# Performance work log

Hardware: AMD Instinct MI355X
Metric: run time of the kernel (lower is better)

The kernel has to match this reference:

```python
import jax, jax.numpy as jnp
import numpy as np

B_BOUND = 3.0
K = 10
SCALE_DIM = 8
TOTAL_DIM = 16
HID = 50
N = 262144
TD = TOTAL_DIM - SCALE_DIM  # transform_dim


def setup_inputs() -> dict:
    key = jax.random.key(0)
    ks = jax.random.split(key, 7)
    s = 0.1  # small init so softmax/softplus params stay well-conditioned
    return {
        "x": jax.random.normal(ks[0], (N, TOTAL_DIM), dtype=jnp.float32),
        "w0": s * jax.random.normal(ks[1], (SCALE_DIM, HID), dtype=jnp.float32),
        "b0": jnp.zeros((HID,), jnp.float32),
        "w1": s * jax.random.normal(ks[2], (HID, HID), dtype=jnp.float32),
        "b1": jnp.zeros((HID,), jnp.float32),
        "ww": s * jax.random.normal(ks[3], (HID, TD * K), dtype=jnp.float32),
        "bw": jnp.zeros((TD * K,), jnp.float32),
        "wh": s * jax.random.normal(ks[4], (HID, TD * K), dtype=jnp.float32),
        "bh": jnp.zeros((TD * K,), jnp.float32),
        "wd": s * jax.random.normal(ks[5], (HID, TD * (K - 1)), dtype=jnp.float32),
        "bd": jnp.zeros((TD * (K - 1),), jnp.float32),
    }


def _spline_forward(x, w0, b0, w1, b1, ww, bw, wh, bh, wd, bd):
    B = B_BOUND
    zd = x[:, :SCALE_DIM]          # conditioner input [N, d]
    u = x[:, SCALE_DIM:]           # values to transform [N, D]
    n, D = u.shape

    h = jnp.tanh(zd @ w0 + b0)
    h = jnp.tanh(h @ w1 + b1)

    theta_w = jax.nn.softmax((2.0 * B * (h @ ww + bw)).reshape(n, D, K), axis=-1)
    theta_h = jax.nn.softmax((2.0 * B * (h @ wh + bh)).reshape(n, D, K), axis=-1)
    theta_d = jax.nn.softplus((h @ wd + bd).reshape(n, D, K - 1))

    # Bin edges in [-B, B] via cumsum of normalized widths/heights
    xe = jnp.concatenate(
        [jnp.full((n, D, 1), -B, u.dtype), -B + 2.0 * B * jnp.cumsum(theta_w, axis=-1)], axis=-1)  # [n,D,K+1]
    ye = jnp.concatenate(
        [jnp.full((n, D, 1), -B, u.dtype), -B + 2.0 * B * jnp.cumsum(theta_h, axis=-1)], axis=-1)
    # Knot derivatives: boundary derivatives fixed to 1 (linear tails)
    ones = jnp.ones((n, D, 1), u.dtype)
    d = jnp.concatenate([ones, theta_d, ones], axis=-1)  # [n,D,K+1]

    widths = xe[..., 1:] - xe[..., :-1]
    heights = ye[..., 1:] - ye[..., :-1]

    inside = (u > -B) & (u < B)
    uc = jnp.clip(u, -B, B)
    # per-element bin search
    idx = jnp.clip(jnp.sum((uc[..., None] >= xe[..., :-1]).astype(jnp.int32), axis=-1) - 1, 0, K - 1)
    idx = idx[..., None]
    take = lambda a: jnp.take_along_axis(a, idx, axis=-1)[..., 0]

    xk, yk = take(xe[..., :-1]), take(ye[..., :-1])
    wk, hk = take(widths), take(heights)
    dk, dk1 = take(d[..., :-1]), take(d[..., 1:])

    sk = hk / wk
    xi = (uc - xk) / wk
    om = 1.0 - xi
    denom = sk + (dk1 + dk - 2.0 * sk) * xi * om
    y = yk + hk * (sk * xi * xi + dk * xi * om) / denom
    logdet = 2.0 * jnp.log(sk) + jnp.log(dk1 * xi * xi + 2.0 * sk * xi * om + dk * om * om) - 2.0 * jnp.log(denom)

    zD = jnp.where(inside, y, u)
    ld = jnp.where(inside, logdet, 0.0)
    return jnp.concatenate([zd, zD], axis=1), jnp.sum(ld)


def reference(x, w0, b0, w1, b1, ww, bw, wh, bh, wd, bd):
    return _spline_forward(x, w0, b0, w1, b1, ww, bw, wh, bh, wd, bd)
```

## Files before the change

kernel.cpp:

```cpp
#include <hip/hip_runtime.h>

#define NROWS 262144
#define KK 10
#define BB 3.0f
#define SROW 132
#define HS 84
#define SEGF16 (16 * SROW)
#define SENT 0.54132485f

typedef _Float16 v8h __attribute__((ext_vector_type(8)));
typedef _Float16 v4h __attribute__((ext_vector_type(4)));
typedef float v4f __attribute__((ext_vector_type(4)));

#define W0_OFF 0
#define W1_OFF 256
#define WC_OFF 768
#define FRAG_TOTAL 2816
#define SLOTS_OFF (FRAG_TOTAL * 4)

#if __has_builtin(__builtin_amdgcn_exp2f)
__device__ __forceinline__ float ex2(float x) { return __builtin_amdgcn_exp2f(x); }
#else
__device__ __forceinline__ float ex2(float x) { return __expf(0.6931471805599453f * x); }
#endif
#if __has_builtin(__builtin_amdgcn_rcpf)
__device__ __forceinline__ float frcp(float x) { return __builtin_amdgcn_rcpf(x); }
#else
__device__ __forceinline__ float frcp(float x) { return __fdividef(1.0f, x); }
#endif

#define LOG2E 1.4426950408889634f
#define C6 (6.0f * LOG2E)
#define CT (2.0f * LOG2E)

__device__ __forceinline__ float fast_tanh(float a) {
    const float e = ex2(CT * a);
    return fmaf(-2.0f, frcp(e + 1.0f), 1.0f);
}

__device__ __forceinline__ float softplus1(float v) {
    return fmaxf(v, 0.0f) + __logf(1.0f + ex2(-LOG2E * fabsf(v)));
}

__device__ __forceinline__ void spline_task(
    const _Float16* __restrict__ sg, int base, float ud, int g, int d,
    float* __restrict__ out, float& ldacc)
{
    float vals[32];
    #pragma unroll
    for (int blk = 0; blk < 8; ++blk) {
        const v4h p = *(const v4h*)&sg[base + blk * 4];
        vals[4 * blk + 0] = (float)p[0];
        vals[4 * blk + 1] = (float)p[1];
        vals[4 * blk + 2] = (float)p[2];
        vals[4 * blk + 3] = (float)p[3];
    }

    float mw = vals[0];
    #pragma unroll
    for (int i = 1; i < KK; ++i) mw = fmaxf(mw, vals[i]);
    const float mw8 = mw * C6;
    float sw = 0.0f;
    #pragma unroll
    for (int i = 0; i < KK; ++i) { vals[i] = ex2(fmaf(vals[i], C6, -mw8)); sw += vals[i]; }
    const float invw = frcp(sw);

    float mh = vals[10];
    #pragma unroll
    for (int i = 1; i < KK; ++i) mh = fmaxf(mh, vals[10 + i]);
    const float mh8 = mh * C6;
    float sh = 0.0f;
    #pragma unroll
    for (int i = 0; i < KK; ++i) { vals[10 + i] = ex2(fmaf(vals[10 + i], C6, -mh8)); sh += vals[10 + i]; }
    const float invh = frcp(sh);

    const float uc = fminf(fmaxf(ud, -BB), BB);
    const bool inside = (ud > -BB) && (ud < BB);

    float cw = 0.0f, ch = 0.0f;
    float xprev = -BB, yprev = -BB, rprev = SENT;
    float xk = -BB, yk = -BB, wk = 1.0f, hk2 = 1.0f, rdk = SENT, rdk1 = SENT;
    #pragma unroll
    for (int i = 0; i < KK; ++i) {
        cw += vals[i] * invw;
        ch += vals[10 + i] * invh;
        const float xnext = fmaf(6.0f, cw, -BB);
        const float ynext = fmaf(6.0f, ch, -BB);
        const float rnext = (i == KK - 1) ? SENT : vals[20 + i];
        const bool c = (i == 0) || (uc >= xprev);
        if (c) { xk = xprev; yk = yprev; wk = xnext - xprev; hk2 = ynext - yprev; rdk = rprev; rdk1 = rnext; }
        xprev = xnext; yprev = ynext; rprev = rnext;
    }
    const float dk = softplus1(rdk);
    const float dk1 = softplus1(rdk1);

    const float rwk = frcp(wk);
    const float sk = hk2 * rwk;
    const float xi = (uc - xk) * rwk;
    const float om = 1.0f - xi;
    const float denom = sk + (dk1 + dk - 2.0f * sk) * xi * om;
    const float rden = frcp(denom);
    const float ynum = sk * xi * xi + dk * xi * om;
    const float yv = yk + hk2 * ynum * rden;
    const float larg = dk1 * xi * xi + 2.0f * sk * xi * om + dk * om * om;
    const float ldet = __logf(sk * sk * larg * rden * rden);

    out[g * 16 + 8 + d] = inside ? yv : ud;
    ldacc += inside ? ldet : 0.0f;
}

__global__ __launch_bounds__(256) void nsf_prep(
    const float* __restrict__ w0, const float* __restrict__ b0,
    const float* __restrict__ w1, const float* __restrict__ b1,
    const float* __restrict__ ww, const float* __restrict__ bw,
    const float* __restrict__ wh, const float* __restrict__ bh,
    const float* __restrict__ wd, const float* __restrict__ bd,
    v8h* __restrict__ wsv, float* __restrict__ wsf)
{
    const int t = blockIdx.x * 256 + threadIdx.x;
    if (t < 64) wsf[SLOTS_OFF + t] = 0.0f;
    if (t >= FRAG_TOTAL) return;

    v8h v;
    #pragma unroll
    for (int j = 0; j < 8; ++j) v[j] = (_Float16)0.0f;

    if (t < W1_OFF) {
        const int tile = t >> 6, lane = t & 63, q = lane >> 4, n = tile * 16 + (lane & 15);
        if (n < 50) {
            #pragma unroll
            for (int j = 0; j < 8; ++j) {
                const int k = q * 8 + j;
                if (k < 8)       v[j] = (_Float16)w0[k * 50 + n];
                else if (k == 8) v[j] = (_Float16)b0[n];
            }
        }
    } else if (t < WC_OFF) {
        int p = t - W1_OFF;
        const int step = p >> 8; p &= 255;
        const int tile = p >> 6, lane = p & 63, q = lane >> 4, n = tile * 16 + (lane & 15);
        if (n < 50) {
            #pragma unroll
            for (int j = 0; j < 8; ++j) {
                const int k = step * 32 + q * 8 + j;
                if (k < 50)       v[j] = (_Float16)w1[k * 50 + n];
                else if (k == 50) v[j] = (_Float16)b1[n];
            }
        }
    } else {
        int p = t - WC_OFF;
        const int step = p >> 10; p &= 1023;
        const int tile = p >> 6, lane = p & 63, q = lane >> 4;
        const int cp = tile * 16 + (lane & 15);
        const int d = cp >> 5, jj = cp & 31;
        #pragma unroll
        for (int j = 0; j < 8; ++j) {
            const int k = step * 32 + q * 8 + j;
            float val = 0.0f;
            if (k < 50) {
                if (jj < 10)      val = ww[k * 80 + d * 10 + jj];
                else if (jj < 20) val = wh[k * 80 + d * 10 + (jj - 10)];
                else if (jj < 29) val = wd[k * 72 + d * 9 + (jj - 20)];
            } else if (k == 50) {
                if (jj < 10)      val = bw[d * 10 + jj];
                else if (jj < 20) val = bh[d * 10 + (jj - 10)];
                else if (jj < 29) val = bd[d * 9 + (jj - 20)];
            }
            v[j] = (_Float16)val;
        }
    }
    wsv[t] = v;
}

__global__ __launch_bounds__(128) void nsf_main_v8(
    const float* __restrict__ x,
    const v8h* __restrict__ wsv,
    float* __restrict__ out, float* __restrict__ slots)
{
    __shared__ __align__(16) _Float16 smem[4 * SEGF16];
    const int w = threadIdx.x >> 6;
    const int lane = threadIdx.x & 63;
    const int q = lane >> 4, l15 = lane & 15;
    _Float16* segA = &smem[(2 * w) * SEGF16];
    _Float16* segB = &smem[(2 * w + 1) * SEGF16];
    const int waveId = blockIdx.x * 2 + w;
    const int R0 = waveId * 32;

    const float4* xv = (const float4*)x;
    float4* ov = (float4*)out;

    const float uA0 = x[(R0 + l15) * 16 + 8 + q];
    const float uA1 = x[(R0 + l15) * 16 + 12 + q];
    const float uB0 = x[(R0 + 16 + l15) * 16 + 8 + q];
    const float uB1 = x[(R0 + 16 + l15) * 16 + 12 + q];

    {
        const int gg = R0 + (lane >> 1);
        const int part = lane & 1;
        ov[gg * 4 + part] = xv[gg * 4 + part];
    }

    v8h aA, aB;
    #pragma unroll
    for (int j = 0; j < 8; ++j) { aA[j] = (_Float16)0.0f; aB[j] = (_Float16)0.0f; }
    if (lane < 16) {
        const float4 f0 = xv[(R0 + lane) * 4 + 0];
        const float4 f1 = xv[(R0 + lane) * 4 + 1];
        aA[0] = (_Float16)f0.x; aA[1] = (_Float16)f0.y; aA[2] = (_Float16)f0.z; aA[3] = (_Float16)f0.w;
        aA[4] = (_Float16)f1.x; aA[5] = (_Float16)f1.y; aA[6] = (_Float16)f1.z; aA[7] = (_Float16)f1.w;
        const float4 g0 = xv[(R0 + 16 + lane) * 4 + 0];
        const float4 g1 = xv[(R0 + 16 + lane) * 4 + 1];
        aB[0] = (_Float16)g0.x; aB[1] = (_Float16)g0.y; aB[2] = (_Float16)g0.z; aB[3] = (_Float16)g0.w;
        aB[4] = (_Float16)g1.x; aB[5] = (_Float16)g1.y; aB[6] = (_Float16)g1.z; aB[7] = (_Float16)g1.w;
    }
    if (q == 1) { aA[0] = (_Float16)1.0f; aB[0] = (_Float16)1.0f; }

    #pragma unroll
    for (int t = 0; t < 4; ++t) {
        const v8h b = wsv[W0_OFF + t * 64 + lane];
        v4f cA = __builtin_amdgcn_mfma_f32_16x16x32_f16(b, aA, (v4f)(0.0f), 0, 0, 0);
        v4f cB = __builtin_amdgcn_mfma_f32_16x16x32_f16(b, aB, (v4f)(0.0f), 0, 0, 0);
        v4h pA, pB;
        #pragma unroll
        for (int rg = 0; rg < 4; ++rg) {
            pA[rg] = (_Float16)fast_tanh(cA[rg]);
            pB[rg] = (_Float16)fast_tanh(cB[rg]);
        }
        const int o = l15 * HS + t * 16 + q * 4;
        *(v4h*)&segA[o] = pA;
        *(v4h*)&segB[o] = pB;
    }

    v8h A0A, A1A, A0B, A1B;
    {
        const int o0 = l15 * HS + q * 8;
        const int o1 = l15 * HS + 32 + q * 8;
        const v4h a0l = *(const v4h*)&segA[o0], a0h = *(const v4h*)&segA[o0 + 4];
        const v4h a1l = *(const v4h*)&segA[o1], a1h = *(const v4h*)&segA[o1 + 4];
        const v4h b0l = *(const v4h*)&segB[o0], b0h = *(const v4h*)&segB[o0 + 4];
        const v4h b1l = *(const v4h*)&segB[o1], b1h = *(const v4h*)&segB[o1 + 4];
        #pragma unroll
        for (int j = 0; j < 4; ++j) {
            A0A[j] = a0l[j]; A0A[4 + j] = a0h[j];
            A1A[j] = a1l[j]; A1A[4 + j] = a1h[j];
            A0B[j] = b0l[j]; A0B[4 + j] = b0h[j];
            A1B[j] = b1l[j]; A1B[4 + j] = b1h[j];
        }
    }
    if (q == 2) { A1A[2] = (_Float16)1.0f; A1B[2] = (_Float16)1.0f; }
    #pragma unroll
    for (int t = 0; t < 4; ++t) {
        const v8h bf0 = wsv[W1_OFF + t * 64 + lane];
        const v8h bf1 = wsv[W1_OFF + 256 + t * 64 + lane];
        v4f cA = __builtin_amdgcn_mfma_f32_16x16x32_f16(bf0, A0A, (v4f)(0.0f), 0, 0, 0);
        cA = __builtin_amdgcn_mfma_f32_16x16x32_f16(bf1, A1A, cA, 0, 0, 0);
        v4f cB = __builtin_amdgcn_mfma_f32_16x16x32_f16(bf0, A0B, (v4f)(0.0f), 0, 0, 0);
        cB = __builtin_amdgcn_mfma_f32_16x16x32_f16(bf1, A1B, cB, 0, 0, 0);
        v4h pA, pB;
        #pragma unroll
        for (int rg = 0; rg < 4; ++rg) {
            pA[rg] = (_Float16)fast_tanh(cA[rg]);
            pB[rg] = (_Float16)fast_tanh(cB[rg]);
        }
        const int o = l15 * HS + t * 16 + q * 4;
        *(v4h*)&segA[o] = pA;
        *(v4h*)&segB[o] = pB;
    }

    {
        const int o0 = l15 * HS + q * 8;
        const int o1 = l15 * HS + 32 + q * 8;
        const v4h a0l = *(const v4h*)&segA[o0], a0h = *(const v4h*)&segA[o0 + 4];
        const v4h a1l = *(const v4h*)&segA[o1], a1h = *(const v4h*)&segA[o1 + 4];
        const v4h b0l = *(const v4h*)&segB[o0], b0h = *(const v4h*)&segB[o0 + 4];
        const v4h b1l = *(const v4h*)&segB[o1], b1h = *(const v4h*)&segB[o1 + 4];
        #pragma unroll
        for (int j = 0; j < 4; ++j) {
            A0A[j] = a0l[j]; A0A[4 + j] = a0h[j];
            A1A[j] = a1l[j]; A1A[4 + j] = a1h[j];
            A0B[j] = b0l[j]; A0B[4 + j] = b0h[j];
            A1B[j] = b1l[j]; A1B[4 + j] = b1h[j];
        }
    }
    if (q == 2) { A1A[2] = (_Float16)1.0f; A1B[2] = (_Float16)1.0f; }

    float ldacc = 0.0f;

    #pragma unroll 2
    for (int t = 0; t < 8; ++t) {
        const v8h bf0 = wsv[WC_OFF + t * 64 + lane];
        const v8h bf1 = wsv[WC_OFF + 1024 + t * 64 + lane];
        v4f cA = __builtin_amdgcn_mfma_f32_16x16x32_f16(bf0, A0A, (v4f)(0.0f), 0, 0, 0);
        cA = __builtin_amdgcn_mfma_f32_16x16x32_f16(bf1, A1A, cA, 0, 0, 0);
        v4f cB = __builtin_amdgcn_mfma_f32_16x16x32_f16(bf0, A0B, (v4f)(0.0f), 0, 0, 0);
        cB = __builtin_amdgcn_mfma_f32_16x16x32_f16(bf1, A1B, cB, 0, 0, 0);
        v4h pA, pB;
        #pragma unroll
        for (int rg = 0; rg < 4; ++rg) { pA[rg] = (_Float16)cA[rg]; pB[rg] = (_Float16)cB[rg]; }
        const int o = l15 * SROW + t * 16 + q * 4;
        *(v4h*)&segA[o] = pA;
        *(v4h*)&segB[o] = pB;
    }

    spline_task(segA, l15 * SROW + q * 32, uA0, R0 + l15, q, out, ldacc);
    spline_task(segB, l15 * SROW + q * 32, uB0, R0 + 16 + l15, q, out, ldacc);

    #pragma unroll 2
    for (int t = 8; t < 16; ++t) {
        const v8h bf0 = wsv[WC_OFF + t * 64 + lane];
        const v8h bf1 = wsv[WC_OFF + 1024 + t * 64 + lane];
        v4f cA = __builtin_amdgcn_mfma_f32_16x16x32_f16(bf0, A0A, (v4f)(0.0f), 0, 0, 0);
        cA = __builtin_amdgcn_mfma_f32_16x16x32_f16(bf1, A1A, cA, 0, 0, 0);
        v4f cB = __builtin_amdgcn_mfma_f32_16x16x32_f16(bf0, A0B, (v4f)(0.0f), 0, 0, 0);
        cB = __builtin_amdgcn_mfma_f32_16x16x32_f16(bf1, A1B, cB, 0, 0, 0);
        v4h pA, pB;
        #pragma unroll
        for (int rg = 0; rg < 4; ++rg) { pA[rg] = (_Float16)cA[rg]; pB[rg] = (_Float16)cB[rg]; }
        const int o = l15 * SROW + (t - 8) * 16 + q * 4;
        *(v4h*)&segA[o] = pA;
        *(v4h*)&segB[o] = pB;
    }

    spline_task(segA, l15 * SROW + q * 32, uA1, R0 + l15, q + 4, out, ldacc);
    spline_task(segB, l15 * SROW + q * 32, uB1, R0 + 16 + l15, q + 4, out, ldacc);

    #pragma unroll
    for (int off = 32; off > 0; off >>= 1) ldacc += __shfl_down(ldacc, off);
    if (lane == 0) atomicAdd(&slots[waveId & 63], ldacc);
}

__global__ void nsf_finish(const float* __restrict__ slots, float* __restrict__ ldp) {
    float v = slots[threadIdx.x];
    #pragma unroll
    for (int off = 32; off > 0; off >>= 1) v += __shfl_down(v, off);
    if (threadIdx.x == 0) *ldp = v;
}

extern "C" void kernel_launch(void* const* d_in, const int* in_sizes, int n_in,
                              void* d_out, int out_size, void* d_ws, size_t ws_size,
                              hipStream_t stream) {
    const float* x  = (const float*)d_in[0];
    const float* w0 = (const float*)d_in[1];
    const float* b0 = (const float*)d_in[2];
    const float* w1 = (const float*)d_in[3];
    const float* b1 = (const float*)d_in[4];
    const float* ww = (const float*)d_in[5];
    const float* bw = (const float*)d_in[6];
    const float* wh = (const float*)d_in[7];
    const float* bh = (const float*)d_in[8];
    const float* wd = (const float*)d_in[9];
    const float* bd = (const float*)d_in[10];

    float* out = (float*)d_out;
    float* ldp = out + (size_t)NROWS * 16;
    v8h* wsv = (v8h*)d_ws;
    float* wsf = (float*)d_ws;
    float* slots = wsf + SLOTS_OFF;

    hipLaunchKernelGGL(nsf_prep, dim3((FRAG_TOTAL + 255) / 256), dim3(256), 0, stream,
                       w0, b0, w1, b1, ww, bw, wh, bh, wd, bd, wsv, wsf);
    hipLaunchKernelGGL(nsf_main_v8, dim3(NROWS / 64), dim3(128), 0, stream,
                       x, wsv, out, slots);
    hipLaunchKernelGGL(nsf_finish, dim3(1), dim3(64), 0, stream, slots, ldp);
}
```

Before: 155.5 us.

## Stage weight fragments in LDS and coalesce u loads/output stores via LDS

Each 256-thread block now cooperatively copies all MFMA weight fragments from global memory into LDS once, and the MFMA loops read B operands from LDS instead of global/L2. The u columns are loaded as coalesced float4 rows, staged through LDS, and the transformed outputs are written back as full float4 rows instead of scattered 4-byte stores. Block size doubles to four waves, amortizing the weight copy. The cost is about 45KB of LDS per block for fragments, which may limit occupancy, plus an added block-wide barrier.

```diff
diff --git a/kernel.cpp b/kernel.cpp
--- a/kernel.cpp
+++ b/kernel.cpp
@@ -42,9 +42,8 @@
     return fmaxf(v, 0.0f) + __logf(1.0f + ex2(-LOG2E * fabsf(v)));
 }
 
-__device__ __forceinline__ void spline_task(
-    const _Float16* __restrict__ sg, int base, float ud, int g, int d,
-    float* __restrict__ out, float& ldacc)
+__device__ __forceinline__ float spline_task(
+    const _Float16* __restrict__ sg, int base, float ud, float& ldacc)
 {
     float vals[32];
     #pragma unroll
@@ -105,8 +104,8 @@
     const float larg = dk1 * xi * xi + 2.0f * sk * xi * om + dk * om * om;
     const float ldet = __logf(sk * sk * larg * rden * rden);
 
-    out[g * 16 + 8 + d] = inside ? yv : ud;
     ldacc += inside ? ldet : 0.0f;
+    return inside ? yv : ud;
 }
 
 __global__ __launch_bounds__(256) void nsf_prep(
@@ -172,33 +171,45 @@
     wsv[t] = v;
 }
 
-__global__ __launch_bounds__(128) void nsf_main_v8(
+__global__ __launch_bounds__(256) void nsf_main_v10(
     const float* __restrict__ x,
     const v8h* __restrict__ wsv,
     float* __restrict__ out, float* __restrict__ slots)
 {
-    __shared__ __align__(16) _Float16 smem[4 * SEGF16];
+    __shared__ __align__(16) v8h fragLDS[FRAG_TOTAL];
+    __shared__ __align__(16) _Float16 segAll[4 * 2 * SEGF16];
     const int w = threadIdx.x >> 6;
     const int lane = threadIdx.x & 63;
     const int q = lane >> 4, l15 = lane & 15;
-    _Float16* segA = &smem[(2 * w) * SEGF16];
-    _Float16* segB = &smem[(2 * w + 1) * SEGF16];
-    const int waveId = blockIdx.x * 2 + w;
+    _Float16* segA = &segAll[w * 2 * SEGF16];
+    _Float16* segB = segA + SEGF16;
+    float* uz = (float*)segA;
+    const int waveId = blockIdx.x * 4 + w;
     const int R0 = waveId * 32;
 
     const float4* xv = (const float4*)x;
     float4* ov = (float4*)out;
 
-    const float uA0 = x[(R0 + l15) * 16 + 8 + q];
-    const float uA1 = x[(R0 + l15) * 16 + 12 + q];
-    const float uB0 = x[(R0 + 16 + l15) * 16 + 8 + q];
-    const float uB1 = x[(R0 + 16 + l15) * 16 + 12 + q];
-
     {
-        const int gg = R0 + (lane >> 1);
-        const int part = lane & 1;
-        ov[gg * 4 + part] = xv[gg * 4 + part];
-    }
+        const int base = w * (FRAG_TOTAL / 4);
+        #pragma unroll
+        for (int r = 0; r < 11; ++r) {
+            const int i = base + r * 64 + lane;
+            fragLDS[i] = wsv[i];
+        }
+    }
+
+    const int pr = lane >> 1, pc = lane & 1;
+    {
+        const float4 p01 = xv[(R0 + pr) * 4 + pc];
+        ov[(R0 + pr) * 4 + pc] = p01;
+        const float4 p23 = xv[(R0 + pr) * 4 + 2 + pc];
+        *(float4*)&uz[pr * 8 + pc * 4] = p23;
+    }
+    const float uA0 = uz[l15 * 8 + q];
+    const float uA1 = uz[l15 * 8 + 4 + q];
+    const float uB0 = uz[(16 + l15) * 8 + q];
+    const float uB1 = uz[(16 + l15) * 8 + 4 + q];
 
     v8h aA, aB;
     #pragma unroll
@@ -215,9 +226,11 @@
     }
     if (q == 1) { aA[0] = (_Float16)1.0f; aB[0] = (_Float16)1.0f; }
 
+    __syncthreads();
+
     #pragma unroll
     for (int t = 0; t < 4; ++t) {
-        const v8h b = wsv[W0_OFF + t * 64 + lane];
+        const v8h b = fragLDS[W0_OFF + t * 64 + lane];
         v4f cA = __builtin_amdgcn_mfma_f32_16x16x32_f16(b, aA, (v4f)(0.0f), 0, 0, 0);
         v4f cB = __builtin_amdgcn_mfma_f32_16x16x32_f16(b, aB, (v4f)(0.0f), 0, 0, 0);
         v4h pA, pB;
@@ -250,8 +263,8 @@
     if (q == 2) { A1A[2] = (_Float16)1.0f; A1B[2] = (_Float16)1.0f; }
     #pragma unroll
     for (int t = 0; t < 4; ++t) {
-        const v8h bf0 = wsv[W1_OFF + t * 64 + lane];
-        const v8h bf1 = wsv[W1_OFF + 256 + t * 64 + lane];
+        const v8h bf0 = fragLDS[W1_OFF + t * 64 + lane];
+        const v8h bf1 = fragLDS[W1_OFF + 256 + t * 64 + lane];
         v4f cA = __builtin_amdgcn_mfma_f32_16x16x32_f16(bf0, A0A, (v4f)(0.0f), 0, 0, 0);
         cA = __builtin_amdgcn_mfma_f32_16x16x32_f16(bf1, A1A, cA, 0, 0, 0);
         v4f cB = __builtin_amdgcn_mfma_f32_16x16x32_f16(bf0, A0B, (v4f)(0.0f), 0, 0, 0);
@@ -288,8 +301,8 @@
 
     #pragma unroll 2
     for (int t = 0; t < 8; ++t) {
-        const v8h bf0 = wsv[WC_OFF + t * 64 + lane];
-        const v8h bf1 = wsv[WC_OFF + 1024 + t * 64 + lane];
+        const v8h bf0 = fragLDS[WC_OFF + t * 64 + lane];
+        const v8h bf1 = fragLDS[WC_OFF + 1024 + t * 64 + lane];
         v4f cA = __builtin_amdgcn_mfma_f32_16x16x32_f16(bf0, A0A, (v4f)(0.0f), 0, 0, 0);
         cA = __builtin_amdgcn_mfma_f32_16x16x32_f16(bf1, A1A, cA, 0, 0, 0);
         v4f cB = __builtin_amdgcn_mfma_f32_16x16x32_f16(bf0, A0B, (v4f)(0.0f), 0, 0, 0);
@@ -302,13 +315,13 @@
         *(v4h*)&segB[o] = pB;
     }
 
-    spline_task(segA, l15 * SROW + q * 32, uA0, R0 + l15, q, out, ldacc);
-    spline_task(segB, l15 * SROW + q * 32, uB0, R0 + 16 + l15, q, out, ldacc);
+    const float zA0 = spline_task(segA, l15 * SROW + q * 32, uA0, ldacc);
+    const float zB0 = spline_task(segB, l15 * SROW + q * 32, uB0, ldacc);
 
     #pragma unroll 2
     for (int t = 8; t < 16; ++t) {
-        const v8h bf0 = wsv[WC_OFF + t * 64 + lane];
-        const v8h bf1 = wsv[WC_OFF + 1024 + t * 64 + lane];
+        const v8h bf0 = fragLDS[WC_OFF + t * 64 + lane];
+        const v8h bf1 = fragLDS[WC_OFF + 1024 + t * 64 + lane];
         v4f cA = __builtin_amdgcn_mfma_f32_16x16x32_f16(bf0, A0A, (v4f)(0.0f), 0, 0, 0);
         cA = __builtin_amdgcn_mfma_f32_16x16x32_f16(bf1, A1A, cA, 0, 0, 0);
         v4f cB = __builtin_amdgcn_mfma_f32_16x16x32_f16(bf0, A0B, (v4f)(0.0f), 0, 0, 0);
@@ -321,8 +334,14 @@
         *(v4h*)&segB[o] = pB;
     }
 
-    spline_task(segA, l15 * SROW + q * 32, uA1, R0 + l15, q + 4, out, ldacc);
-    spline_task(segB, l15 * SROW + q * 32, uB1, R0 + 16 + l15, q + 4, out, ldacc);
+    const float zA1 = spline_task(segA, l15 * SROW + q * 32, uA1, ldacc);
+    const float zB1 = spline_task(segB, l15 * SROW + q * 32, uB1, ldacc);
+
+    uz[l15 * 8 + q]            = zA0;
+    uz[l15 * 8 + 4 + q]        = zA1;
+    uz[(16 + l15) * 8 + q]     = zB0;
+    uz[(16 + l15) * 8 + 4 + q] = zB1;
+    ov[(R0 + pr) * 4 + 2 + pc] = *(const float4*)&uz[pr * 8 + pc * 4];
 
     #pragma unroll
     for (int off = 32; off > 0; off >>= 1) ldacc += __shfl_down(ldacc, off);
@@ -359,7 +378,7 @@
 
     hipLaunchKernelGGL(nsf_prep, dim3((FRAG_TOTAL + 255) / 256), dim3(256), 0, stream,
                        w0, b0, w1, b1, ww, bw, wh, bh, wd, bd, wsv, wsf);
-    hipLaunchKernelGGL(nsf_main_v8, dim3(NROWS / 64), dim3(128), 0, stream,
+    hipLaunchKernelGGL(nsf_main_v10, dim3(NROWS / 128), dim3(256), 0, stream,
                        x, wsv, out, slots);
     hipLaunchKernelGGL(nsf_finish, dim3(1), dim3(64), 0, stream, slots, ldp);
 }
```

Result: no change. 152.5 us (-1.9%).
